# Performance work log

Hardware: AMD Instinct MI355X
Metric: run time of the kernel (lower is better)

## Reference

```python
import jax, jax.numpy as jnp
import numpy as np

N = 5000        # nodes
F = 7699        # node feature dim (fixed by code)
E = 40000       # edges
ED = 3          # edge_dim (fixed by code)
H1, C1 = 4, 1024
H2, C2 = 1, 1024
NUM_OUT = 128
NEG_SLOPE = 0.2


def _glorot(key, shape):
    fan_in = shape[0]
    return jax.random.normal(key, shape, jnp.float32) / np.float32(np.sqrt(fan_in))


def setup_inputs() -> dict:
    key = jax.random.key(0)
    ks = jax.random.split(key, 16)
    x = jax.random.normal(ks[0], (N, F), jnp.float32)
    src = jax.random.randint(ks[1], (E,), 0, N)
    dst = jax.random.randint(ks[2], (E,), 0, N)
    src = jnp.where(src == dst, (src + 1) % N, src)  # no pre-existing self loops
    edge_index = jnp.stack([src, dst]).astype(jnp.int32)
    edge_attr = jax.random.normal(ks[3], (E, ED), jnp.float32)
    inp = {
        "x": x, "edge_index": edge_index, "edge_attr": edge_attr,
        # GATv2Conv #1: 7699 -> 1024, heads=4, edge_dim=3
        "W1l": _glorot(ks[4], (F, H1 * C1)), "b1l": jnp.zeros((H1 * C1,), jnp.float32),
        "W1r": _glorot(ks[5], (F, H1 * C1)), "b1r": jnp.zeros((H1 * C1,), jnp.float32),
        "W1e": _glorot(ks[6], (ED, H1 * C1)),
        "att1": _glorot(ks[7], (H1, C1)),
        "bias1": jnp.zeros((H1 * C1,), jnp.float32),
        # GATv2Conv #2: 4096 -> 1024, heads=1, edge_dim=3
        "W2l": _glorot(ks[8], (H1 * C1, H2 * C2)), "b2l": jnp.zeros((H2 * C2,), jnp.float32),
        "W2r": _glorot(ks[9], (H1 * C1, H2 * C2)), "b2r": jnp.zeros((H2 * C2,), jnp.float32),
        "W2e": _glorot(ks[10], (ED, H2 * C2)),
        "att2": _glorot(ks[11], (H2, C2)),
        "bias2": jnp.zeros((H2 * C2,), jnp.float32),
        # final Linear(1024, num_outputs)
        "Wlin": _glorot(ks[12], (C2, NUM_OUT)), "blin": jnp.zeros((NUM_OUT,), jnp.float32),
    }
    return inp


def gatv2_layer(x, src, dst, edge_attr, Wl, bl, Wr, br, We, att, bias, heads, out_ch):
    """PyG GATv2Conv with add_self_loops=True, fill_value='mean', concat=True."""
    n = x.shape[0]
    # self-loop edge_attr = mean of incoming edge attrs per node (fill_value='mean')
    deg = jax.ops.segment_sum(jnp.ones((src.shape[0],), jnp.float32), dst, num_segments=n)
    loop_attr = jax.ops.segment_sum(edge_attr, dst, num_segments=n) / jnp.maximum(deg, 1.0)[:, None]
    idx = jnp.arange(n, dtype=src.dtype)
    srcf = jnp.concatenate([src, idx])
    dstf = jnp.concatenate([dst, idx])
    ea = jnp.concatenate([edge_attr, loop_attr], axis=0)
    xl = (x @ Wl + bl).reshape(n, heads, out_ch)   # lin_l (source)
    xr = (x @ Wr + br).reshape(n, heads, out_ch)   # lin_r (target)
    ee = (ea @ We).reshape(-1, heads, out_ch)       # lin_edge (no bias)
    e = jax.nn.leaky_relu(xl[srcf] + xr[dstf] + ee, NEG_SLOPE)  # [E', H, C]
    logit = jnp.einsum('ehc,hc->eh', e, att)                     # [E', H]
    # segment softmax over destination nodes (every node has a self loop)
    m = jax.lax.stop_gradient(jax.ops.segment_max(logit, dstf, num_segments=n))
    a = jnp.exp(logit - m[dstf])
    denom = jax.ops.segment_sum(a, dstf, num_segments=n)
    alpha = a / (denom[dstf] + 1e-16)
    out = jax.ops.segment_sum(alpha[:, :, None] * xl[srcf], dstf, num_segments=n)  # [N,H,C]
    return out.reshape(n, heads * out_ch) + bias


def reference(x, edge_index, edge_attr,
              W1l, b1l, W1r, b1r, W1e, att1, bias1,
              W2l, b2l, W2r, b2r, W2e, att2, bias2,
              Wlin, blin):
    src, dst = edge_index[0], edge_index[1]
    h = gatv2_layer(x, src, dst, edge_attr, W1l, b1l, W1r, b1r, W1e, att1, bias1, H1, C1)
    h = gatv2_layer(h, src, dst, edge_attr, W2l, b2l, W2r, b2r, W2e, att2, bias2, H2, C2)
    return h @ Wlin + blin
```

## Files before the change

### kernel.cpp

```cpp
#include <hip/hip_runtime.h>
#include <cstdint>
#include <cstddef>

#define N_NODES 5000
#define F_IN    7699
#define KP1     7712
#define KT1     241
#define MP      5120
#define E_EDGES 40000
#define EFULL   45000
#define HC1     4096
#define N1      8192
#define HC2     1024
#define N2      2048
#define NOUT    128

typedef __bf16 bf16x8 __attribute__((ext_vector_type(8)));
typedef float  f32x4  __attribute__((ext_vector_type(4)));
typedef float  f32x16 __attribute__((ext_vector_type(16)));
typedef unsigned short u16x8 __attribute__((ext_vector_type(8)));
typedef _Float16 f16;
typedef _Float16 f16x8 __attribute__((ext_vector_type(8)));

using as1_uchar = unsigned char __attribute__((address_space(1)));
using as3_uchar = unsigned char __attribute__((address_space(3)));

__device__ __forceinline__ unsigned short f2bf(float f) {
  union { float f; unsigned int u; } v; v.f = f;
  return (unsigned short)((v.u + 0x7fffu + ((v.u >> 16) & 1u)) >> 16);
}
__device__ __forceinline__ float bf2f(unsigned short h) {
  union { unsigned int u; float f; } v; v.u = ((unsigned int)h) << 16;
  return v.f;
}

__device__ __forceinline__ void gload16(const void* g, void* l) {
  __builtin_amdgcn_global_load_lds(
      reinterpret_cast<const as1_uchar*>(reinterpret_cast<uintptr_t>(g)),
      reinterpret_cast<as3_uchar*>(reinterpret_cast<uintptr_t>(l)),
      16, 0, 0);
}



__global__ void k_split_x(const float* __restrict__ x, unsigned short* __restrict__ hi,
                          unsigned short* __restrict__ lo) {
  const int C8 = KP1 / 8;
  int ci = blockIdx.x * 256 + threadIdx.x;
  if (ci >= MP * C8) return;
  int r = ci / C8, c8 = ci % C8;
  int c = c8 * 8;
  u16x8 hb, lb;
  #pragma unroll
  for (int j = 0; j < 8; ++j) {
    float v = 0.f;
    if (r < N_NODES && (c + j) < F_IN) v = x[(size_t)r * F_IN + c + j];
    unsigned short h = f2bf(v);
    hb[j] = h; lb[j] = f2bf(v - bf2f(h));
  }
  size_t off = ((size_t)((r >> 7) * KT1 + (c >> 5)) * 4 + ((c >> 3) & 3)) * 1024 + (r & 127) * 8;
  *(u16x8*)&hi[off] = hb;
  *(u16x8*)&lo[off] = lb;
}


__global__ void k_split_w(const float* __restrict__ W,
                          unsigned short* __restrict__ hi, unsigned short* __restrict__ lo,
                          int K, int Nsrc, int c0, int KT, int rowOffset) {
  __shared__ float tile[32][33];
  const int tid = threadIdx.x;
  const int kt = blockIdx.x;
  const int n0 = blockIdx.y * 32;
  #pragma unroll
  for (int i = tid >> 5; i < 32; i += 8) {
    int k = kt * 32 + i;
    tile[i][tid & 31] = (k < K) ? W[(size_t)k * Nsrc + c0 + n0 + (tid & 31)] : 0.f;
  }
  __syncthreads();
  if (tid < 128) {
    const int nn = tid >> 2, kc = (tid & 3) << 3;
    const int n = rowOffset + n0 + nn;
    u16x8 hb, lb;
    #pragma unroll
    for (int j = 0; j < 8; ++j) {
      float v = tile[kc + j][nn];
      unsigned short h = f2bf(v);
      hb[j] = h; lb[j] = f2bf(v - bf2f(h));
    }
    size_t off = ((size_t)((n >> 7) * KT + kt) * 4 + (kc >> 3)) * 1024 + (n & 127) * 8;
    *(u16x8*)&hi[off] = hb;
    *(u16x8*)&lo[off] = lb;
  }
}


template <int OF16>
__global__ __launch_bounds__(256, 3) void k_gemm_bb(
    const unsigned short* __restrict__ Ahi, const unsigned short* __restrict__ Alo,
    const unsigned short* __restrict__ Bhi, const unsigned short* __restrict__ Blo,
    void* __restrict__ Cp, const float* __restrict__ bias0, const float* __restrict__ bias1,
    int halfN, int M, int ldC, int KT, int gm)
{
  __shared__ __align__(16) unsigned short AhS[4096];
  __shared__ __align__(16) unsigned short AlS[4096];
  __shared__ __align__(16) unsigned short BhS[4096];
  __shared__ __align__(16) unsigned short BlS[4096];

  const int tid = threadIdx.x;
  const int lane = tid & 63;
  const int w = tid >> 6;
  const int wm = w >> 1, wn = w & 1;

  const int chunkg = gridDim.x >> 3;
  const int wg = (blockIdx.x & 7) * chunkg + (blockIdx.x >> 3);
  const int bm = wg % gm, bn = wg / gm;

  f32x16 acc[2][2] = {};

  const unsigned short* AbH = Ahi + (size_t)bm * KT * 4096;
  const unsigned short* AbL = Alo + (size_t)bm * KT * 4096;
  const unsigned short* BbH = Bhi + (size_t)bn * KT * 4096;
  const unsigned short* BbL = Blo + (size_t)bn * KT * 4096;
  const int sOff = w * 1024 + lane * 8;

  const int r5 = lane & 31, h5 = lane >> 5;

  auto stage = [&](int kt) {
    const size_t o = (size_t)kt * 4096 + sOff;
    gload16(AbH + o,       &AhS[w * 1024]);
    gload16(AbH + o + 512, &AhS[w * 1024 + 512]);
    gload16(AbL + o,       &AlS[w * 1024]);
    gload16(AbL + o + 512, &AlS[w * 1024 + 512]);
    gload16(BbH + o,       &BhS[w * 1024]);
    gload16(BbH + o + 512, &BhS[w * 1024 + 512]);
    gload16(BbL + o,       &BlS[w * 1024]);
    gload16(BbL + o + 512, &BlS[w * 1024 + 512]);
  };

  stage(0);
  __syncthreads();

  for (int kt = 0; kt < KT; ++kt) {
    bf16x8 ah[2][2], al[2][2];
    #pragma unroll
    for (int i = 0; i < 2; ++i)
      #pragma unroll
      for (int kh = 0; kh < 2; ++kh) {
        const int ro = (kh * 2 + h5) * 1024 + (wm * 64 + i * 32 + r5) * 8;
        ah[i][kh] = *(const bf16x8*)&AhS[ro];
        al[i][kh] = *(const bf16x8*)&AlS[ro];
      }
    __builtin_amdgcn_s_setprio(1);
    #pragma unroll
    for (int j = 0; j < 2; ++j) {
      #pragma unroll
      for (int kh = 0; kh < 2; ++kh) {
        const int ro = (kh * 2 + h5) * 1024 + (wn * 64 + j * 32 + r5) * 8;
        bf16x8 bh = *(const bf16x8*)&BhS[ro];
        bf16x8 bl = *(const bf16x8*)&BlS[ro];
        #pragma unroll
        for (int i = 0; i < 2; ++i) {
          acc[i][j] = __builtin_amdgcn_mfma_f32_32x32x16_bf16(ah[i][kh], bh, acc[i][j], 0, 0, 0);
          acc[i][j] = __builtin_amdgcn_mfma_f32_32x32x16_bf16(al[i][kh], bh, acc[i][j], 0, 0, 0);
          acc[i][j] = __builtin_amdgcn_mfma_f32_32x32x16_bf16(ah[i][kh], bl, acc[i][j], 0, 0, 0);
        }
      }
    }
    __builtin_amdgcn_s_setprio(0);
    __syncthreads();
    if (kt + 1 < KT) stage(kt + 1);
    __syncthreads();
  }

  #pragma unroll
  for (int i = 0; i < 2; ++i) {
    #pragma unroll
    for (int j = 0; j < 2; ++j) {
      const int gc = bn * 128 + wn * 64 + j * 32 + r5;
      const float bv = (gc < halfN) ? bias0[gc] : bias1[gc - halfN];
      #pragma unroll
      for (int reg = 0; reg < 16; ++reg) {
        const int gr = bm * 128 + wm * 64 + i * 32 + (reg & 3) + 8 * (reg >> 2) + 4 * h5;
        if (gr < M) {
          float v = acc[i][j][reg] + bv;
          if (OF16) ((f16*)Cp)[(size_t)gr * ldC + gc] = (f16)v;
          else      ((float*)Cp)[(size_t)gr * ldC + gc] = v;
        }
      }
    }
  }
}


__global__ void k_deg(const int* __restrict__ dst, const float* __restrict__ ea,
                      float* __restrict__ deg, float* __restrict__ lattr, int E) {
  int e = blockIdx.x * 256 + threadIdx.x;
  if (e >= E) return;
  int d = dst[e];
  atomicAdd(&deg[d], 1.f);
  atomicAdd(&lattr[d * 3 + 0], ea[e * 3 + 0]);
  atomicAdd(&lattr[d * 3 + 1], ea[e * 3 + 1]);
  atomicAdd(&lattr[d * 3 + 2], ea[e * 3 + 2]);
}

__global__ void k_lattr_fin(float* __restrict__ lattr, const float* __restrict__ deg, int n) {
  int i = blockIdx.x * 256 + threadIdx.x;
  if (i >= n) return;
  float dv = fmaxf(deg[i], 1.f);
  lattr[i * 3 + 0] /= dv; lattr[i * 3 + 1] /= dv; lattr[i * 3 + 2] /= dv;
}

__global__ void k_eafull(const float* __restrict__ ea, const float* __restrict__ lattr,
                         float* __restrict__ eaf, int E, int n) {
  int e = blockIdx.x * 256 + threadIdx.x;
  if (e >= E + n) return;
  const float* s = (e < E) ? &ea[(size_t)e * 3] : &lattr[(size_t)(e - E) * 3];
  eaf[e * 3 + 0] = s[0]; eaf[e * 3 + 1] = s[1]; eaf[e * 3 + 2] = s[2];
}

__global__ void k_count(const int* __restrict__ dst, int* __restrict__ cnt, int E, int n) {
  int e = blockIdx.x * 256 + threadIdx.x;
  if (e >= E + n) return;
  int d = (e < E) ? dst[e] : (e - E);
  atomicAdd(&cnt[d], 1);
}

__global__ void k_scan(const int* __restrict__ cnt, int* __restrict__ rowptr, int n) {
  int lane = threadIdx.x;
  int run = 0;
  for (int base = 0; base < n; base += 64) {
    int i = base + lane;
    int v = (i < n) ? cnt[i] : 0;
    #pragma unroll
    for (int off = 1; off < 64; off <<= 1) {
      int t = __shfl_up(v, off, 64);
      if (lane >= off) v += t;
    }
    if (i < n) rowptr[i + 1] = run + v;
    run += __shfl(v, 63, 64);
  }
  if (lane == 0) rowptr[0] = 0;
}

__global__ void k_fill(const int* __restrict__ dst, const int* __restrict__ rowptr,
                       int* __restrict__ fillc, int* __restrict__ elist, int E, int n) {
  int e = blockIdx.x * 256 + threadIdx.x;
  if (e >= E + n) return;
  int d = (e < E) ? dst[e] : (e - E);
  int pos = rowptr[d] + atomicAdd(&fillc[d], 1);
  elist[pos] = e;
}


template <int H, int ITERS>
__global__ __launch_bounds__(256) void k_logit(
    const f16* __restrict__ xl, const f16* __restrict__ xr, int strideX,
    const float* __restrict__ eaf, const float* __restrict__ We, const float* __restrict__ att,
    const int* __restrict__ src, const int* __restrict__ dst, int E,
    float* __restrict__ logit)
{
  const int e = blockIdx.x;
  const int tid = threadIdx.x;
  int s, d;
  if (e < E) { s = src[e]; d = dst[e]; } else { s = e - E; d = s; }
  const float ea0 = eaf[e * 3 + 0], ea1 = eaf[e * 3 + 1], ea2 = eaf[e * 3 + 2];
  constexpr int HC = ITERS * 256;
  const f16* rl = xl + (size_t)s * strideX;
  const f16* rr = xr + (size_t)d * strideX;
  float acc[H];
  #pragma unroll
  for (int h = 0; h < H; ++h) acc[h] = 0.f;
  #pragma unroll
  for (int i = 0; i < ITERS; ++i) {
    int hc = tid + (i << 8);
    float v = (float)rl[hc] + (float)rr[hc]
            + ea0 * We[hc] + ea1 * We[HC + hc] + ea2 * We[2 * HC + hc];
    v = (v > 0.f) ? v : 0.2f * v;
    acc[i >> 2] += v * att[hc];
  }
  __shared__ float red[H][4];
  const int lane = tid & 63, wv = tid >> 6;
  #pragma unroll
  for (int h = 0; h < H; ++h) {
    float v = acc[h];
    #pragma unroll
    for (int off = 32; off > 0; off >>= 1) v += __shfl_down(v, off, 64);
    if (lane == 0) red[h][wv] = v;
  }
  __syncthreads();
  if (tid < H)
    logit[(size_t)e * H + tid] = red[tid][0] + red[tid][1] + red[tid][2] + red[tid][3];
}

template <int H>
__global__ void k_stats(const float* __restrict__ logit, const int* __restrict__ rowptr,
                        const int* __restrict__ elist, float* __restrict__ mb, float* __restrict__ db)
{
  const int n = blockIdx.x;
  const int lane = threadIdx.x;
  const int start = rowptr[n], end = rowptr[n + 1];
  #pragma unroll
  for (int h = 0; h < H; ++h) {
    float m = -1e30f;
    for (int p = start + lane; p < end; p += 64)
      m = fmaxf(m, logit[(size_t)elist[p] * H + h]);
    #pragma unroll
    for (int off = 32; off > 0; off >>= 1) m = fmaxf(m, __shfl_down(m, off, 64));
    m = __shfl(m, 0, 64);
    float sum = 0.f;
    for (int p = start + lane; p < end; p += 64)
      sum += __expf(logit[(size_t)elist[p] * H + h] - m);
    #pragma unroll
    for (int off = 32; off > 0; off >>= 1) sum += __shfl_down(sum, off, 64);
    if (lane == 0) { mb[n * H + h] = m; db[n * H + h] = sum; }
  }
}

template <int H, int NC8, int KTo>
__global__ __launch_bounds__(256) void k_agg(
    const f16* __restrict__ xl, int strideX,
    const int* __restrict__ rowptr, const int* __restrict__ elist, const int* __restrict__ src,
    const float* __restrict__ logit, const float* __restrict__ mb, const float* __restrict__ db,
    const float* __restrict__ bias,
    unsigned short* __restrict__ ohi, unsigned short* __restrict__ olo, int E)
{
  const int n = blockIdx.x;
  const int tid = threadIdx.x;
  constexpr int HC = H * 1024;
  float acc[NC8][8];
  #pragma unroll
  for (int q = 0; q < NC8; ++q)
    #pragma unroll
    for (int j = 0; j < 8; ++j) acc[q][j] = 0.f;
  const int start = rowptr[n], end = rowptr[n + 1];
  float mloc[H], dloc[H];
  #pragma unroll
  for (int h = 0; h < H; ++h) { mloc[h] = mb[n * H + h]; dloc[h] = db[n * H + h] + 1e-16f; }
  for (int p = start; p < end; ++p) {
    const int e = elist[p];
    const int s = (e < E) ? src[e] : (e - E);
    float al[H];
    #pragma unroll
    for (int h = 0; h < H; ++h)
      al[h] = __expf(logit[(size_t)e * H + h] - mloc[h]) / dloc[h];
    const f16* row = xl + (size_t)s * strideX;
    #pragma unroll
    for (int q = 0; q < NC8; ++q) {
      const int c8 = tid + q * 256;
      if (c8 * 8 < HC) {
        float a = (H == 4) ? ((tid & 128) ? al[2 * q + 1] : al[2 * q]) : al[0];
        f16x8 v = *(const f16x8*)(row + c8 * 8);
        #pragma unroll
        for (int j = 0; j < 8; ++j) acc[q][j] += a * (float)v[j];
      }
    }
  }
  #pragma unroll
  for (int q = 0; q < NC8; ++q) {
    const int c8 = tid + q * 256;
    if (c8 * 8 < HC) {
      u16x8 hb, lb;
      #pragma unroll
      for (int j = 0; j < 8; ++j) {
        float v = acc[q][j] + bias[c8 * 8 + j];
        unsigned short h = f2bf(v);
        hb[j] = h; lb[j] = f2bf(v - bf2f(h));
      }
      size_t off = ((size_t)((n >> 7) * KTo + (c8 >> 2)) * 4 + (c8 & 3)) * 1024 + (n & 127) * 8;
      *(u16x8*)&ohi[off] = hb;
      *(u16x8*)&olo[off] = lb;
    }
  }
}


extern "C" void kernel_launch(void* const* d_in, const int* in_sizes, int n_in,
                              void* d_out, int out_size, void* d_ws, size_t ws_size,
                              hipStream_t stream) {
  const float* x    = (const float*)d_in[0];
  const int*   eidx = (const int*)d_in[1];
  const float* eattr= (const float*)d_in[2];
  const float* W1l  = (const float*)d_in[3];
  const float* b1l  = (const float*)d_in[4];
  const float* W1r  = (const float*)d_in[5];
  const float* b1r  = (const float*)d_in[6];
  const float* W1e  = (const float*)d_in[7];
  const float* att1 = (const float*)d_in[8];
  const float* bias1= (const float*)d_in[9];
  const float* W2l  = (const float*)d_in[10];
  const float* b2l  = (const float*)d_in[11];
  const float* W2r  = (const float*)d_in[12];
  const float* b2r  = (const float*)d_in[13];
  const float* W2e  = (const float*)d_in[14];
  const float* att2 = (const float*)d_in[15];
  const float* bias2= (const float*)d_in[16];
  const float* Wlin = (const float*)d_in[17];
  const float* blin = (const float*)d_in[18];
  float* out = (float*)d_out;

  char* ws = (char*)d_ws;
  const int* srcp = eidx;
  const int* dstp = eidx + E_EDGES;

  auto alignup = [](size_t v) { return (v + 255) & ~(size_t)255; };

  const size_t oXHI = 0;
  const size_t oXLO = oXHI + (size_t)MP * KP1 * 2;
  const size_t oXLR = oXLO + (size_t)MP * KP1 * 2;
  const size_t oBH  = oXLR + (size_t)N_NODES * N1 * 2;
  const size_t oBL  = oBH + (size_t)4096 * KP1 * 2;
  const size_t oS   = oBL + (size_t)4096 * KP1 * 2;
  const size_t oLATTR = alignup(oS);
  const size_t oDEG   = alignup(oLATTR + (size_t)N_NODES * 3 * 4);
  const size_t oEAF   = alignup(oDEG + (size_t)N_NODES * 4);
  const size_t oCNT   = alignup(oEAF + (size_t)EFULL * 3 * 4);
  const size_t oROW   = alignup(oCNT + (size_t)N_NODES * 4);
  const size_t oFILL  = alignup(oROW + (size_t)(N_NODES + 1) * 4);
  const size_t oELIST = alignup(oFILL + (size_t)N_NODES * 4);
  const size_t oLOGIT = alignup(oELIST + (size_t)EFULL * 4);
  const size_t oMB    = alignup(oLOGIT + (size_t)EFULL * 4 * 4);
  const size_t oDB    = alignup(oMB + (size_t)N_NODES * 4 * 4);
  const size_t oEND   = alignup(oDB + (size_t)N_NODES * 4 * 4);
  if (ws_size < oEND) return;

  const size_t oH1HI = oXHI;
  const size_t oH1LO = oXLO;
  const size_t oXLR2 = oXLR;
  const size_t oH2HI = oXLR + 32ull * 1024 * 1024;
  const size_t oH2LO = oXLR + 48ull * 1024 * 1024;
  const size_t oB2H  = oBH;
  const size_t oB2L  = oBL;
  const size_t oB3H  = oBH;
  const size_t oB3L  = oBH + 1ull * 1024 * 1024;

  unsigned short* XHI  = (unsigned short*)(ws + oXHI);
  unsigned short* XLO  = (unsigned short*)(ws + oXLO);
  f16*            XLR  = (f16*)(ws + oXLR);
  unsigned short* BH   = (unsigned short*)(ws + oBH);
  unsigned short* BL   = (unsigned short*)(ws + oBL);
  float*          LATTR= (float*)(ws + oLATTR);
  float*          DEG  = (float*)(ws + oDEG);
  float*          EAF  = (float*)(ws + oEAF);
  int*            CNT  = (int*)(ws + oCNT);
  int*            ROWP = (int*)(ws + oROW);
  int*            FILLC= (int*)(ws + oFILL);
  int*            ELIST= (int*)(ws + oELIST);
  float*          LOGIT= (float*)(ws + oLOGIT);
  float*          MB   = (float*)(ws + oMB);
  float*          DB   = (float*)(ws + oDB);
  unsigned short* H1HI = (unsigned short*)(ws + oH1HI);
  unsigned short* H1LO = (unsigned short*)(ws + oH1LO);
  f16*            XLR2 = (f16*)(ws + oXLR2);
  unsigned short* H2HI = (unsigned short*)(ws + oH2HI);
  unsigned short* H2LO = (unsigned short*)(ws + oH2LO);
  unsigned short* B2H  = (unsigned short*)(ws + oB2H);
  unsigned short* B2L  = (unsigned short*)(ws + oB2L);
  unsigned short* B3H  = (unsigned short*)(ws + oB3H);
  unsigned short* B3L  = (unsigned short*)(ws + oB3L);

  hipMemsetAsync(ws + oDEG,   0, (size_t)N_NODES * 4, stream);
  hipMemsetAsync(ws + oLATTR, 0, (size_t)N_NODES * 3 * 4, stream);
  hipMemsetAsync(ws + oCNT,   0, (size_t)N_NODES * 4, stream);
  hipMemsetAsync(ws + oFILL,  0, (size_t)N_NODES * 4, stream);

  const int gE  = (E_EDGES + 255) / 256;
  const int gEF = (EFULL + 255) / 256;
  const int gN  = (N_NODES + 255) / 256;

  k_deg<<<gE, 256, 0, stream>>>(dstp, eattr, DEG, LATTR, E_EDGES);
  k_lattr_fin<<<gN, 256, 0, stream>>>(LATTR, DEG, N_NODES);
  k_eafull<<<gEF, 256, 0, stream>>>(eattr, LATTR, EAF, E_EDGES, N_NODES);
  k_count<<<gEF, 256, 0, stream>>>(dstp, CNT, E_EDGES, N_NODES);
  k_scan<<<1, 64, 0, stream>>>(CNT, ROWP, N_NODES);
  k_fill<<<gEF, 256, 0, stream>>>(dstp, ROWP, FILLC, ELIST, E_EDGES, N_NODES);

  k_split_x<<<MP * (KP1 / 8) / 256, 256, 0, stream>>>(x, XHI, XLO);

  k_split_w<<<dim3(KT1, HC1 / 32), 256, 0, stream>>>(W1l, BH, BL, F_IN, HC1, 0, KT1, 0);
  k_gemm_bb<1><<<(HC1 / 128) * (MP / 128), 256, 0, stream>>>(
      XHI, XLO, BH, BL, XLR, b1l, b1l, HC1, N_NODES, N1, KT1, MP / 128);

  k_split_w<<<dim3(KT1, HC1 / 32), 256, 0, stream>>>(W1r, BH, BL, F_IN, HC1, 0, KT1, 0);
  k_gemm_bb<1><<<(HC1 / 128) * (MP / 128), 256, 0, stream>>>(
      XHI, XLO, BH, BL, XLR + HC1, b1r, b1r, HC1, N_NODES, N1, KT1, MP / 128);

  k_logit<4, 16><<<EFULL, 256, 0, stream>>>(XLR, XLR + HC1, N1, EAF, W1e, att1, srcp, dstp, E_EDGES, LOGIT);
  k_stats<4><<<N_NODES, 64, 0, stream>>>(LOGIT, ROWP, ELIST, MB, DB);
  hipMemsetAsync(ws + oH1HI, 0, (size_t)MP * HC1 * 2, stream);
  hipMemsetAsync(ws + oH1LO, 0, (size_t)MP * HC1 * 2, stream);
  k_agg<4, 2, HC1 / 32><<<N_NODES, 256, 0, stream>>>(
      XLR, N1, ROWP, ELIST, srcp, LOGIT, MB, DB, bias1, H1HI, H1LO, E_EDGES);

  k_split_w<<<dim3(HC1 / 32, HC2 / 32), 256, 0, stream>>>(W2l, B2H, B2L, HC1, HC2, 0, HC1 / 32, 0);
  k_split_w<<<dim3(HC1 / 32, HC2 / 32), 256, 0, stream>>>(W2r, B2H, B2L, HC1, HC2, 0, HC1 / 32, HC2);
  k_gemm_bb<1><<<(N2 / 128) * (MP / 128), 256, 0, stream>>>(
      H1HI, H1LO, B2H, B2L, XLR2, b2l, b2r, HC2, N_NODES, N2, HC1 / 32, MP / 128);

  k_logit<1, 4><<<EFULL, 256, 0, stream>>>(XLR2, XLR2 + HC2, N2, EAF, W2e, att2, srcp, dstp, E_EDGES, LOGIT);
  k_stats<1><<<N_NODES, 64, 0, stream>>>(LOGIT, ROWP, ELIST, MB, DB);
  hipMemsetAsync(ws + oH2HI, 0, (size_t)MP * HC2 * 2, stream);
  hipMemsetAsync(ws + oH2LO, 0, (size_t)MP * HC2 * 2, stream);
  k_agg<1, 1, HC2 / 32><<<N_NODES, 256, 0, stream>>>(
      XLR2, N2, ROWP, ELIST, srcp, LOGIT, MB, DB, bias2, H2HI, H2LO, E_EDGES);

  k_split_w<<<dim3(HC2 / 32, NOUT / 32), 256, 0, stream>>>(Wlin, B3H, B3L, HC2, NOUT, 0, HC2 / 32, 0);
  k_gemm_bb<0><<<(NOUT / 128) * (MP / 128), 256, 0, stream>>>(
      H2HI, H2LO, B3H, B3L, out, blin, blin, NOUT, N_NODES, NOUT, HC2 / 32, MP / 128);
}
```

Baseline: 2.997 ms.

## Double-buffer GEMM LDS tiles with prefetch two steps ahead and band-swizzle blocks

The split-bf16 GEMM now keeps two LDS stages and issues global-to-LDS loads for step kt+2 while MFMAs run on the current buffer. The two full syncthreads per step become explicit waitcnt/barrier pairs. Block-to-tile mapping changes to bands of 8 M-tiles that sweep every N-tile, which should improve L2 reuse of A. LDS use doubles, so launch bounds drop from 3 to 2 blocks per CU, which may lower occupancy.

```diff
diff --git a/kernel.cpp b/kernel.cpp
--- a/kernel.cpp
+++ b/kernel.cpp
@@ -95,25 +95,27 @@
 
 
 template <int OF16>
-__global__ __launch_bounds__(256, 3) void k_gemm_bb(
+__global__ __launch_bounds__(256, 2) void k_gemm_bb(
     const unsigned short* __restrict__ Ahi, const unsigned short* __restrict__ Alo,
     const unsigned short* __restrict__ Bhi, const unsigned short* __restrict__ Blo,
     void* __restrict__ Cp, const float* __restrict__ bias0, const float* __restrict__ bias1,
-    int halfN, int M, int ldC, int KT, int gm)
+    int halfN, int M, int ldC, int KT, int gn)
 {
-  __shared__ __align__(16) unsigned short AhS[4096];
-  __shared__ __align__(16) unsigned short AlS[4096];
-  __shared__ __align__(16) unsigned short BhS[4096];
-  __shared__ __align__(16) unsigned short BlS[4096];
+  __shared__ __align__(16) unsigned short AhS[2 * 4096];
+  __shared__ __align__(16) unsigned short AlS[2 * 4096];
+  __shared__ __align__(16) unsigned short BhS[2 * 4096];
+  __shared__ __align__(16) unsigned short BlS[2 * 4096];
 
   const int tid = threadIdx.x;
   const int lane = tid & 63;
   const int w = tid >> 6;
   const int wm = w >> 1, wn = w & 1;
 
-  const int chunkg = gridDim.x >> 3;
-  const int wg = (blockIdx.x & 7) * chunkg + (blockIdx.x >> 3);
-  const int bm = wg % gm, bn = wg / gm;
+  const int s = blockIdx.x;
+  const int band = s / (8 * gn);
+  const int r = s % (8 * gn);
+  const int bn = r >> 3;
+  const int bm = band * 8 + (r & 7);
 
   f32x16 acc[2][2] = {};
 
@@ -125,51 +127,63 @@
 
   const int r5 = lane & 31, h5 = lane >> 5;
 
-  auto stage = [&](int kt) {
+  auto stage = [&](int kt, int p) {
     const size_t o = (size_t)kt * 4096 + sOff;
-    gload16(AbH + o,       &AhS[w * 1024]);
-    gload16(AbH + o + 512, &AhS[w * 1024 + 512]);
-    gload16(AbL + o,       &AlS[w * 1024]);
-    gload16(AbL + o + 512, &AlS[w * 1024 + 512]);
-    gload16(BbH + o,       &BhS[w * 1024]);
-    gload16(BbH + o + 512, &BhS[w * 1024 + 512]);
-    gload16(BbL + o,       &BlS[w * 1024]);
-    gload16(BbL + o + 512, &BlS[w * 1024 + 512]);
+    const int lp = p * 4096 + w * 1024;
+    gload16(AbH + o,       &AhS[lp]);
+    gload16(AbH + o + 512, &AhS[lp + 512]);
+    gload16(AbL + o,       &AlS[lp]);
+    gload16(AbL + o + 512, &AlS[lp + 512]);
+    gload16(BbH + o,       &BhS[lp]);
+    gload16(BbH + o + 512, &BhS[lp + 512]);
+    gload16(BbL + o,       &BlS[lp]);
+    gload16(BbL + o + 512, &BlS[lp + 512]);
   };
 
-  stage(0);
-  __syncthreads();
+  stage(0, 0);
+  stage(1, 1);
+  asm volatile("s_waitcnt vmcnt(8)" ::: "memory");
+  __builtin_amdgcn_s_barrier();
 
   for (int kt = 0; kt < KT; ++kt) {
-    bf16x8 ah[2][2], al[2][2];
+    const int p = kt & 1;
+    bf16x8 ah[2][2], al[2][2], bh[2][2], bl[2][2];
     #pragma unroll
     for (int i = 0; i < 2; ++i)
       #pragma unroll
       for (int kh = 0; kh < 2; ++kh) {
-        const int ro = (kh * 2 + h5) * 1024 + (wm * 64 + i * 32 + r5) * 8;
+        const int ro = p * 4096 + (kh * 2 + h5) * 1024 + (wm * 64 + i * 32 + r5) * 8;
         ah[i][kh] = *(const bf16x8*)&AhS[ro];
         al[i][kh] = *(const bf16x8*)&AlS[ro];
       }
-    __builtin_amdgcn_s_setprio(1);
-    #pragma unroll
-    for (int j = 0; j < 2; ++j) {
+    #pragma unroll
+    for (int j = 0; j < 2; ++j)
       #pragma unroll
       for (int kh = 0; kh < 2; ++kh) {
-        const int ro = (kh * 2 + h5) * 1024 + (wn * 64 + j * 32 + r5) * 8;
-        bf16x8 bh = *(const bf16x8*)&BhS[ro];
-        bf16x8 bl = *(const bf16x8*)&BlS[ro];
+        const int ro = p * 4096 + (kh * 2 + h5) * 1024 + (wn * 64 + j * 32 + r5) * 8;
+        bh[j][kh] = *(const bf16x8*)&BhS[ro];
+        bl[j][kh] = *(const bf16x8*)&BlS[ro];
+      }
+    asm volatile("s_waitcnt lgkmcnt(0)" ::: "memory");
+    __builtin_amdgcn_s_barrier();
+    const int ks = (kt + 2 < KT) ? kt + 2 : KT - 1;
+    stage(ks, p);
+
+    __builtin_amdgcn_s_setprio(1);
+    #pragma unroll
+    for (int j = 0; j < 2; ++j)
+      #pragma unroll
+      for (int kh = 0; kh < 2; ++kh)
         #pragma unroll
         for (int i = 0; i < 2; ++i) {
-          acc[i][j] = __builtin_amdgcn_mfma_f32_32x32x16_bf16(ah[i][kh], bh, acc[i][j], 0, 0, 0);
-          acc[i][j] = __builtin_amdgcn_mfma_f32_32x32x16_bf16(al[i][kh], bh, acc[i][j], 0, 0, 0);
-          acc[i][j] = __builtin_amdgcn_mfma_f32_32x32x16_bf16(ah[i][kh], bl, acc[i][j], 0, 0, 0);
+          acc[i][j] = __builtin_amdgcn_mfma_f32_32x32x16_bf16(ah[i][kh], bh[j][kh], acc[i][j], 0, 0, 0);
+          acc[i][j] = __builtin_amdgcn_mfma_f32_32x32x16_bf16(al[i][kh], bh[j][kh], acc[i][j], 0, 0, 0);
+          acc[i][j] = __builtin_amdgcn_mfma_f32_32x32x16_bf16(ah[i][kh], bl[j][kh], acc[i][j], 0, 0, 0);
         }
-      }
-    }
     __builtin_amdgcn_s_setprio(0);
-    __syncthreads();
-    if (kt + 1 < KT) stage(kt + 1);
-    __syncthreads();
+
+    asm volatile("s_waitcnt vmcnt(8)" ::: "memory");
+    __builtin_amdgcn_s_barrier();
   }
 
   #pragma unroll
@@ -478,11 +492,11 @@
 
   k_split_w<<<dim3(KT1, HC1 / 32), 256, 0, stream>>>(W1l, BH, BL, F_IN, HC1, 0, KT1, 0);
   k_gemm_bb<1><<<(HC1 / 128) * (MP / 128), 256, 0, stream>>>(
-      XHI, XLO, BH, BL, XLR, b1l, b1l, HC1, N_NODES, N1, KT1, MP / 128);
+      XHI, XLO, BH, BL, XLR, b1l, b1l, HC1, N_NODES, N1, KT1, HC1 / 128);
 
   k_split_w<<<dim3(KT1, HC1 / 32), 256, 0, stream>>>(W1r, BH, BL, F_IN, HC1, 0, KT1, 0);
   k_gemm_bb<1><<<(HC1 / 128) * (MP / 128), 256, 0, stream>>>(
-      XHI, XLO, BH, BL, XLR + HC1, b1r, b1r, HC1, N_NODES, N1, KT1, MP / 128);
+      XHI, XLO, BH, BL, XLR + HC1, b1r, b1r, HC1, N_NODES, N1, KT1, HC1 / 128);
 
   k_logit<4, 16><<<EFULL, 256, 0, stream>>>(XLR, XLR + HC1, N1, EAF, W1e, att1, srcp, dstp, E_EDGES, LOGIT);
   k_stats<4><<<N_NODES, 64, 0, stream>>>(LOGIT, ROWP, ELIST, MB, DB);
@@ -494,7 +508,7 @@
   k_split_w<<<dim3(HC1 / 32, HC2 / 32), 256, 0, stream>>>(W2l, B2H, B2L, HC1, HC2, 0, HC1 / 32, 0);
   k_split_w<<<dim3(HC1 / 32, HC2 / 32), 256, 0, stream>>>(W2r, B2H, B2L, HC1, HC2, 0, HC1 / 32, HC2);
   k_gemm_bb<1><<<(N2 / 128) * (MP / 128), 256, 0, stream>>>(
-      H1HI, H1LO, B2H, B2L, XLR2, b2l, b2r, HC2, N_NODES, N2, HC1 / 32, MP / 128);
+      H1HI, H1LO, B2H, B2L, XLR2, b2l, b2r, HC2, N_NODES, N2, HC1 / 32, N2 / 128);
 
   k_logit<1, 4><<<EFULL, 256, 0, stream>>>(XLR2, XLR2 + HC2, N2, EAF, W2e, att2, srcp, dstp, E_EDGES, LOGIT);
   k_stats<1><<<N_NODES, 64, 0, stream>>>(LOGIT, ROWP, ELIST, MB, DB);
@@ -505,5 +519,5 @@
 
   k_split_w<<<dim3(HC2 / 32, NOUT / 32), 256, 0, stream>>>(Wlin, B3H, B3L, HC2, NOUT, 0, HC2 / 32, 0);
   k_gemm_bb<0><<<(NOUT / 128) * (MP / 128), 256, 0, stream>>>(
-      H2HI, H2LO, B3H, B3L, out, blin, blin, NOUT, N_NODES, NOUT, HC2 / 32, MP / 128);
-}
+      H2HI, H2LO, B3H, B3L, out, blin, blin, NOUT, N_NODES, NOUT, HC2 / 32, NOUT / 128);
+}
```

Result: faster. 2.868 ms (-4.3%).
